# Optimization experiments

Measured on AMD Instinct MI355X. Metric: run time of the kernel, lower is better.

The kernel has to match this reference:

```python
import jax, jax.numpy as jnp
import numpy as np

PARENTS = np.array([-1, 0, 1, 1, 1])
NECK_CHAIN = np.array([1, 0])  # neck joint (1) up to root (0)
B, V, F, J, S, E = 512, 5023, 9976, 5, 100, 50
L_STAT, L_DYN, L_FULL, N_BUCKET = 51, 17, 68, 79


def rodrigues(rvec):
    """Axis-angle [N,3] -> rotation matrices [N,3,3]."""
    angle = jnp.linalg.norm(rvec + 1e-8, axis=-1, keepdims=True)  # [N,1]
    axis = rvec / angle
    s = jnp.sin(angle)[..., None]
    c = jnp.cos(angle)[..., None]
    rx, ry, rz = axis[:, 0], axis[:, 1], axis[:, 2]
    z = jnp.zeros_like(rx)
    K = jnp.stack([z, -rz, ry, rz, z, -rx, -ry, rx, z], axis=-1).reshape(-1, 3, 3)
    I = jnp.eye(3, dtype=rvec.dtype)
    return I + s * K + (1.0 - c) * (K @ K)


def verts2lmk(vertices, faces, lmk_faces_idx, lmk_bary):
    lmk_faces = faces[lmk_faces_idx]                               # [B,L,3]
    lmk_verts = jax.vmap(lambda v, f: v[f])(vertices, lmk_faces)   # [B,L,3verts,3xyz]
    return jnp.einsum('blfc,blf->blc', lmk_verts, lmk_bary)


def setup_inputs() -> dict:
    key = jax.random.key(0)
    ks = jax.random.split(key, 16)
    shape_params = jax.random.normal(ks[0], (B, S), jnp.float32)
    expression_params = jax.random.normal(ks[1], (B, E), jnp.float32)
    pose_params = 0.2 * jax.random.normal(ks[2], (B, 6), jnp.float32)
    eye_pose_params = 0.1 * jax.random.normal(ks[3], (B, 6), jnp.float32)
    v_template = jax.random.normal(ks[4], (V, 3), jnp.float32) * 0.1
    shapedirs = jax.random.normal(ks[5], (V, 3, S + E), jnp.float32) * 0.01
    posedirs = jax.random.normal(ks[6], ((J - 1) * 9, V * 3), jnp.float32) * 0.01
    jr = jax.random.uniform(ks[7], (J, V), jnp.float32)
    J_regressor = jr / jnp.sum(jr, axis=1, keepdims=True)
    lbs_weights = jax.nn.softmax(jax.random.normal(ks[8], (V, J), jnp.float32), axis=-1)
    faces = jax.random.randint(ks[9], (F, 3), 0, V)
    lmk_faces_idx = jax.random.randint(ks[10], (L_STAT,), 0, F)
    lb = jax.random.uniform(ks[11], (L_STAT, 3), jnp.float32) + 1e-3
    lmk_bary_coords = lb / jnp.sum(lb, axis=-1, keepdims=True)
    dynamic_lmk_faces_idx = jax.random.randint(ks[12], (N_BUCKET, L_DYN), 0, F)
    db = jax.random.uniform(ks[13], (N_BUCKET, L_DYN, 3), jnp.float32) + 1e-3
    dynamic_lmk_bary_coords = db / jnp.sum(db, axis=-1, keepdims=True)
    full_lmk_faces_idx = jax.random.randint(ks[14], (L_FULL,), 0, F)
    fb = jax.random.uniform(ks[15], (L_FULL, 3), jnp.float32) + 1e-3
    full_lmk_bary_coords = fb / jnp.sum(fb, axis=-1, keepdims=True)
    return {
        'shape_params': shape_params, 'expression_params': expression_params,
        'pose_params': pose_params, 'eye_pose_params': eye_pose_params,
        'v_template': v_template, 'shapedirs': shapedirs, 'posedirs': posedirs,
        'J_regressor': J_regressor, 'lbs_weights': lbs_weights, 'faces': faces,
        'lmk_faces_idx': lmk_faces_idx, 'lmk_bary_coords': lmk_bary_coords,
        'dynamic_lmk_faces_idx': dynamic_lmk_faces_idx,
        'dynamic_lmk_bary_coords': dynamic_lmk_bary_coords,
        'full_lmk_faces_idx': full_lmk_faces_idx,
        'full_lmk_bary_coords': full_lmk_bary_coords,
    }


def reference(shape_params, expression_params, pose_params, eye_pose_params,
              v_template, shapedirs, posedirs, J_regressor, lbs_weights, faces,
              lmk_faces_idx, lmk_bary_coords, dynamic_lmk_faces_idx,
              dynamic_lmk_bary_coords, full_lmk_faces_idx, full_lmk_bary_coords):
    b = shape_params.shape[0]
    nv = v_template.shape[0]
    dt = shape_params.dtype
    betas = jnp.concatenate([shape_params, expression_params], axis=1)          # [B,150]
    neck = jnp.zeros((b, 3), dtype=dt)
    full_pose = jnp.concatenate(
        [pose_params[:, :3], neck, pose_params[:, 3:], eye_pose_params], axis=1)  # [B,15]
    # shape + expression blendshapes
    v_shaped = v_template[None] + jnp.einsum('bl,vcl->bvc', betas, shapedirs)   # [B,V,3]
    joints = jnp.einsum('jv,bvc->bjc', J_regressor, v_shaped)                   # [B,5,3]
    rot_mats = rodrigues(full_pose.reshape(-1, 3)).reshape(b, J, 3, 3)          # [B,5,3,3]
    I3 = jnp.eye(3, dtype=dt)
    pose_feature = (rot_mats[:, 1:] - I3).reshape(b, -1)                        # [B,36]
    v_posed = v_shaped + (pose_feature @ posedirs).reshape(b, nv, 3)
    # kinematic chain -> global joint transforms
    rel_J = joints.at[:, 1:].add(-joints[:, PARENTS[1:]])
    tm = jnp.zeros((b, J, 4, 4), dtype=dt)
    tm = tm.at[:, :, :3, :3].set(rot_mats).at[:, :, :3, 3].set(rel_J).at[:, :, 3, 3].set(1.0)
    chain = [tm[:, 0]]
    for i in range(1, J):
        chain.append(chain[PARENTS[i]] @ tm[:, i])
    A = jnp.stack(chain, axis=1)                                                # [B,5,4,4]
    Rj = jnp.einsum('bjmn,bjn->bjm', A[:, :, :3, :3], joints)
    A_rel = A.at[:, :, :3, 3].add(-Rj)
    # per-vertex skinning
    T = jnp.einsum('vj,bjmn->bvmn', lbs_weights, A_rel)                         # [B,V,4,4]
    vertices = jnp.einsum('bvmn,bvn->bvm', T[:, :, :3, :3], v_posed) + T[:, :, :3, 3]
    # dynamic contour landmark selection from neck kin-chain relative rotation
    aa = full_pose.reshape(b, J, 3)[:, NECK_CHAIN]                              # [B,2,3]
    rc = rodrigues(aa.reshape(-1, 3)).reshape(b, len(NECK_CHAIN), 3, 3)
    rel_rot = jnp.broadcast_to(I3, (b, 3, 3))
    for idx in range(len(NECK_CHAIN)):
        rel_rot = rc[:, idx] @ rel_rot
    sy = jnp.sqrt(rel_rot[:, 0, 0] ** 2 + rel_rot[:, 1, 0] ** 2)
    y_deg = jnp.arctan2(-rel_rot[:, 2, 0], sy) * (180.0 / np.pi)
    y_rot = jnp.round(jnp.minimum(y_deg, 39.0)).astype(jnp.int32)
    neg_mask = y_rot < 0
    big_neg = y_rot < -39
    neg_vals = jnp.where(big_neg, 78, 39 - y_rot)
    y_rot = jnp.where(neg_mask, neg_vals, y_rot)                                # [B] in [0,79)
    dyn_faces = dynamic_lmk_faces_idx[y_rot]                                    # [B,17]
    dyn_bary = dynamic_lmk_bary_coords[y_rot]                                   # [B,17,3]
    lf = jnp.concatenate([dyn_faces, jnp.broadcast_to(lmk_faces_idx[None], (b, lmk_faces_idx.shape[0]))], axis=1)
    lb = jnp.concatenate([dyn_bary, jnp.broadcast_to(lmk_bary_coords[None], (b,) + lmk_bary_coords.shape)], axis=1)
    landmarks2d = verts2lmk(vertices, faces, lf, lb)
    ff = jnp.broadcast_to(full_lmk_faces_idx[None], (b, full_lmk_faces_idx.shape[0]))
    fb = jnp.broadcast_to(full_lmk_bary_coords[None], (b,) + full_lmk_bary_coords.shape)
    landmarks3d = verts2lmk(vertices, faces, ff, fb)
    return (vertices, landmarks2d, landmarks3d)
```

## Files before the change

kernel.cpp:

```cpp
#include <hip/hip_runtime.h>
#include <cstddef>
#include <cstdint>

#define cB   512
#define cV   5023
#define cS   100
#define cE   50
#define cJ   5
#define cLD  17
#define cLF  68

#define cV3    15069
#define cNPAD  15072

#define OUT_V  ((size_t)cB * cV * 3)
#define OUT_L  ((size_t)cB * cLF * 3)

#define WS_BTN    ((size_t)0)
#define WS_ATM    (WS_BTN + (size_t)cNPAD * 96)
#define WS_JS2    (WS_ATM + 49152)
#define WS_AREL   (WS_JS2 + 2432)
#define WS_YROT   (WS_AREL + 30720)
#define WS_JSPART (WS_YROT + 512)

typedef __attribute__((ext_vector_type(8))) short short8;
typedef __attribute__((ext_vector_type(4))) float f32x4;

__device__ __forceinline__ unsigned short f2bf(float x) {
  unsigned int u = __float_as_uint(x);
  u = (u + 0x7fffu + ((u >> 16) & 1u)) >> 16;
  return (unsigned short)u;
}

__device__ __forceinline__ void rodrigues9(float rx, float ry, float rz, float* R) {
  float a0 = rx + 1e-8f, a1 = ry + 1e-8f, a2 = rz + 1e-8f;
  float angle = sqrtf(a0 * a0 + a1 * a1 + a2 * a2);
  float inv = 1.0f / angle;
  float x = rx * inv, y = ry * inv, z = rz * inv;
  float s = sinf(angle), c = cosf(angle);
  float t = 1.0f - c;
  float xy = x * y, xz = x * z, yz = y * z;
  R[0] = 1.0f - t * (y * y + z * z);
  R[1] = -s * z + t * xy;
  R[2] =  s * y + t * xz;
  R[3] =  s * z + t * xy;
  R[4] = 1.0f - t * (x * x + z * z);
  R[5] = -s * x + t * yz;
  R[6] = -s * y + t * xz;
  R[7] =  s * x + t * yz;
  R[8] = 1.0f - t * (x * x + y * y);
}

__global__ __launch_bounds__(512) void k_aux(
    const float* __restrict__ sd, const float* __restrict__ pd,
    const float* __restrict__ jreg, const float* __restrict__ vt,
    unsigned int* __restrict__ btn_u, float* __restrict__ JSpart) {
  __shared__ __align__(16) unsigned char sm[44032];
  float* sdt = (float*)sm;
  unsigned short* pdt = (unsigned short*)(sm + 38912);
  const int t = threadIdx.x;
  const int bid = blockIdx.x;
  if (bid < 314) {
    if (t >= 453) return;
    int c = t / 151, l = t - c * 151;
    int v0 = bid * 16;
    float acc[5] = {0.f, 0.f, 0.f, 0.f, 0.f};
#pragma unroll 8
    for (int vi = 0; vi < 16; ++vi) {
      int v = v0 + vi;
      bool ok = (v < cV);
      int vc = ok ? v : 0;
      float x;
      if (l < 150) x = ok ? sd[(size_t)(v * 3 + c) * 150 + l] : 0.f;
      else         x = ok ? vt[v * 3 + c] : 0.f;
#pragma unroll
      for (int j = 0; j < 5; ++j)
        acc[j] = fmaf(jreg[j * cV + vc], x, acc[j]);
    }
#pragma unroll
    for (int j = 0; j < 5; ++j)
      JSpart[(size_t)bid * 2272 + (j * 3 + c) * 151 + l] = acc[j];
  } else {
    const int n0 = (bid - 314) * 64;
    for (int idx = t; idx < 9600; idx += 512) {
      size_t g = (size_t)n0 * 150 + idx;
      float v = (g < (size_t)cV3 * 150) ? sd[g] : 0.f;
      int row = idx / 150, col = idx - row * 150;
      sdt[row * 152 + col] = v;
    }
    for (int e = t; e < 2304; e += 512) {
      int kk = e >> 6, ln = e & 63;
      int n = n0 + ln;
      pdt[ln * 38 + kk] = f2bf((n < cV3) ? pd[(size_t)kk * cV3 + n] : 0.f);
    }
    __syncthreads();
    for (int e = t; e < 6144; e += 512) {
      int row = e / 96, d = e - row * 96;
      int n = n0 + row;
      if (n < cNPAD) {
        unsigned int wv;
        if (d < 75) {
          wv = (unsigned int)f2bf(sdt[row * 152 + 2 * d]) |
               ((unsigned int)f2bf(sdt[row * 152 + 2 * d + 1]) << 16);
        } else if (d < 93) {
          int p = (d - 75) * 2;
          wv = (unsigned int)pdt[row * 38 + p] |
               ((unsigned int)pdt[row * 38 + p + 1] << 16);
        } else {
          wv = 0u;
        }
        btn_u[(size_t)n * 96 + d] = wv;
      }
    }
  }
}

__global__ __launch_bounds__(256) void k_jsred(const float* __restrict__ JSpart,
                                               float* __restrict__ JS2) {
  __shared__ float red[256];
  const int t = threadIdx.x;
  const int e = blockIdx.x * 32 + (t & 31);
  const int pg = t >> 5;
  float s = 0.f;
  if (e < 2265) {
#pragma unroll 8
    for (int p = pg; p < 314; p += 8)
      s += JSpart[(size_t)p * 2272 + e];
  }
  red[t] = s;
  __syncthreads();
  if (t < 128) red[t] += red[t + 128];
  __syncthreads();
  if (t < 64) red[t] += red[t + 64];
  __syncthreads();
  if (t < 32) {
    float v = red[t] + red[t + 32];
    if (e < 2265) {
      int jc = e / 151, l = e - jc * 151;
      JS2[l * 16 + jc] = v;
    }
  }
}

__global__ __launch_bounds__(256) void k_batch(
    const float* __restrict__ shp, const float* __restrict__ expr,
    const float* __restrict__ pose, const float* __restrict__ eyep,
    const float* __restrict__ JS2g, float* __restrict__ Arel,
    int* __restrict__ yrot, unsigned int* __restrict__ atm_u) {
  __shared__ float js2[151 * 16];
  __shared__ float sb[32 * 153];
  __shared__ float pfs[32 * 36];
  const int t = threadIdx.x;
  const int b0 = blockIdx.x * 32;
  for (int i = t; i < 151 * 16; i += 256) js2[i] = JS2g[i];
  for (int e = t; e < 3200; e += 256) {
    int bl = e / 100, l = e - bl * 100;
    sb[bl * 153 + l] = shp[(size_t)(b0 + bl) * 100 + l];
  }
  for (int e = t; e < 1600; e += 256) {
    int bl = e / 50, l = e - bl * 50;
    sb[bl * 153 + 100 + l] = expr[(size_t)(b0 + bl) * 50 + l];
  }
  __syncthreads();

  if (t < 32) {
    int b = b0 + t;
    float jnt[5][3];
    {
      const f32x4* J4 = (const f32x4*)(js2 + 150 * 16);
      f32x4 A = J4[0], Bq = J4[1], Cq = J4[2], Dq = J4[3];
      jnt[0][0] = A.x;  jnt[0][1] = A.y;  jnt[0][2] = A.z;
      jnt[1][0] = A.w;  jnt[1][1] = Bq.x; jnt[1][2] = Bq.y;
      jnt[2][0] = Bq.z; jnt[2][1] = Bq.w; jnt[2][2] = Cq.x;
      jnt[3][0] = Cq.y; jnt[3][1] = Cq.z; jnt[3][2] = Cq.w;
      jnt[4][0] = Dq.x; jnt[4][1] = Dq.y; jnt[4][2] = Dq.z;
    }
    for (int l = 0; l < 150; ++l) {
      const f32x4* J4 = (const f32x4*)(js2 + l * 16);
      f32x4 A = J4[0], Bq = J4[1], Cq = J4[2], Dq = J4[3];
      float beta = sb[t * 153 + l];
      jnt[0][0] = fmaf(beta, A.x,  jnt[0][0]);
      jnt[0][1] = fmaf(beta, A.y,  jnt[0][1]);
      jnt[0][2] = fmaf(beta, A.z,  jnt[0][2]);
      jnt[1][0] = fmaf(beta, A.w,  jnt[1][0]);
      jnt[1][1] = fmaf(beta, Bq.x, jnt[1][1]);
      jnt[1][2] = fmaf(beta, Bq.y, jnt[1][2]);
      jnt[2][0] = fmaf(beta, Bq.z, jnt[2][0]);
      jnt[2][1] = fmaf(beta, Bq.w, jnt[2][1]);
      jnt[2][2] = fmaf(beta, Cq.x, jnt[2][2]);
      jnt[3][0] = fmaf(beta, Cq.y, jnt[3][0]);
      jnt[3][1] = fmaf(beta, Cq.z, jnt[3][1]);
      jnt[3][2] = fmaf(beta, Cq.w, jnt[3][2]);
      jnt[4][0] = fmaf(beta, Dq.x, jnt[4][0]);
      jnt[4][1] = fmaf(beta, Dq.y, jnt[4][1]);
      jnt[4][2] = fmaf(beta, Dq.z, jnt[4][2]);
    }
    float fp[5][3];
    fp[0][0] = pose[b * 6 + 0]; fp[0][1] = pose[b * 6 + 1]; fp[0][2] = pose[b * 6 + 2];
    fp[1][0] = 0.f; fp[1][1] = 0.f; fp[1][2] = 0.f;
    fp[2][0] = pose[b * 6 + 3]; fp[2][1] = pose[b * 6 + 4]; fp[2][2] = pose[b * 6 + 5];
    fp[3][0] = eyep[b * 6 + 0]; fp[3][1] = eyep[b * 6 + 1]; fp[3][2] = eyep[b * 6 + 2];
    fp[4][0] = eyep[b * 6 + 3]; fp[4][1] = eyep[b * 6 + 4]; fp[4][2] = eyep[b * 6 + 5];
    float R[5][9];
#pragma unroll
    for (int j = 0; j < 5; ++j) rodrigues9(fp[j][0], fp[j][1], fp[j][2], R[j]);
#pragma unroll
    for (int j = 1; j < 5; ++j)
#pragma unroll
      for (int r = 0; r < 9; ++r) {
        float id = (r == 0 || r == 4 || r == 8) ? 1.f : 0.f;
        pfs[t * 36 + (j - 1) * 9 + r] = R[j][r] - id;
      }
    float rel[5][3];
#pragma unroll
    for (int c = 0; c < 3; ++c) {
      rel[0][c] = jnt[0][c];
      rel[1][c] = jnt[1][c] - jnt[0][c];
      rel[2][c] = jnt[2][c] - jnt[1][c];
      rel[3][c] = jnt[3][c] - jnt[1][c];
      rel[4][c] = jnt[4][c] - jnt[1][c];
    }
    float GR[5][9], Gt[5][3];
#pragma unroll
    for (int r = 0; r < 9; ++r) GR[0][r] = R[0][r];
#pragma unroll
    for (int c = 0; c < 3; ++c) Gt[0][c] = rel[0][c];
    const int par[5] = {0, 0, 1, 1, 1};
#pragma unroll
    for (int j = 1; j < 5; ++j) {
      int p = par[j];
#pragma unroll
      for (int r = 0; r < 3; ++r) {
#pragma unroll
        for (int cc = 0; cc < 3; ++cc)
          GR[j][r * 3 + cc] = GR[p][r * 3 + 0] * R[j][0 + cc] +
                              GR[p][r * 3 + 1] * R[j][3 + cc] +
                              GR[p][r * 3 + 2] * R[j][6 + cc];
        Gt[j][r] = Gt[p][r] + GR[p][r * 3 + 0] * rel[j][0] +
                              GR[p][r * 3 + 1] * rel[j][1] +
                              GR[p][r * 3 + 2] * rel[j][2];
      }
    }
#pragma unroll
    for (int j = 0; j < 5; ++j)
#pragma unroll
      for (int r = 0; r < 3; ++r) {
        float tj = Gt[j][r] - (GR[j][r * 3 + 0] * jnt[j][0] +
                               GR[j][r * 3 + 1] * jnt[j][1] +
                               GR[j][r * 3 + 2] * jnt[j][2]);
        Arel[b * 60 + j * 12 + r * 4 + 0] = GR[j][r * 3 + 0];
        Arel[b * 60 + j * 12 + r * 4 + 1] = GR[j][r * 3 + 1];
        Arel[b * 60 + j * 12 + r * 4 + 2] = GR[j][r * 3 + 2];
        Arel[b * 60 + j * 12 + r * 4 + 3] = tj;
      }
    float Ra[9], Rb[9];
    rodrigues9(fp[1][0], fp[1][1], fp[1][2], Ra);
    rodrigues9(fp[0][0], fp[0][1], fp[0][2], Rb);
    float r00 = Rb[0] * Ra[0] + Rb[1] * Ra[3] + Rb[2] * Ra[6];
    float r10 = Rb[3] * Ra[0] + Rb[4] * Ra[3] + Rb[5] * Ra[6];
    float r20 = Rb[6] * Ra[0] + Rb[7] * Ra[3] + Rb[8] * Ra[6];
    float sy = sqrtf(r00 * r00 + r10 * r10);
    float ydeg = atan2f(-r20, sy) * 57.29577951308232f;
    int y = (int)rintf(fminf(ydeg, 39.0f));
    if (y < 0) y = (y < -39) ? 78 : (39 - y);
    yrot[b] = y;
  }
  __syncthreads();

#pragma unroll
  for (int it = 0; it < 12; ++it) {
    int e = t + it * 256;
    int bl = e / 96, d = e - bl * 96;
    unsigned int wv;
    if (d < 75) {
      wv = (unsigned int)f2bf(sb[bl * 153 + 2 * d]) |
           ((unsigned int)f2bf(sb[bl * 153 + 2 * d + 1]) << 16);
    } else if (d < 93) {
      wv = (unsigned int)f2bf(pfs[bl * 36 + (d - 75) * 2]) |
           ((unsigned int)f2bf(pfs[bl * 36 + (d - 75) * 2 + 1]) << 16);
    } else {
      wv = 0u;
    }
    atm_u[(size_t)(b0 + bl) * 96 + d] = wv;
  }
}

__global__ __launch_bounds__(256) void k_main(
    const unsigned short* __restrict__ BTn, const unsigned short* __restrict__ ATm,
    const float* __restrict__ Arel, const float* __restrict__ vtempl,
    const float* __restrict__ lbw, float* __restrict__ out) {
  __shared__ float Pf[96 * 66];
  __shared__ float Os[64 * 97];
  __shared__ float lbwT[160];
  __shared__ float vtT[96];

  const int bid = blockIdx.x;
  const int nb = bid >> 3, mb = bid & 7;

  const int t = threadIdx.x;
  const int w = t >> 6, L = t & 63;
  const int wm = w >> 1, wn = w & 1;
  const int lr = L & 15, lq = L >> 4;

  if (t < 160) {
    int vl = t / 5, j = t - vl * 5;
    int v = nb * 32 + vl;
    lbwT[t] = (v < cV) ? lbw[v * 5 + j] : 0.f;
  }
  if (t >= 160 && t < 256) {
    int e = t - 160;
    int vl = e / 3, c = e - vl * 3;
    int v = nb * 32 + vl;
    vtT[e] = (v < cV) ? vtempl[v * 3 + c] : 0.f;
  }

  const unsigned short* abase = ATm + ((size_t)mb * 64 + wm * 32 + lr) * 192 + lq * 8;
  const unsigned short* bbase = BTn + ((size_t)nb * 96 + wn * 48 + lr) * 192 + lq * 8;

  f32x4 acc[2][3];
#pragma unroll
  for (int mt = 0; mt < 2; ++mt)
#pragma unroll
    for (int nt = 0; nt < 3; ++nt) acc[mt][nt] = (f32x4){0.f, 0.f, 0.f, 0.f};

  short8 af0 = *(const short8*)(abase);
  short8 af1 = *(const short8*)(abase + 16 * 192);
  short8 bf0 = *(const short8*)(bbase);
  short8 bf1 = *(const short8*)(bbase + 16 * 192);
  short8 bf2 = *(const short8*)(bbase + 32 * 192);
#pragma unroll
  for (int ks = 0; ks < 6; ++ks) {
    short8 naf0, naf1, nbf0, nbf1, nbf2;
    if (ks < 5) {
      const int ko = (ks + 1) * 32;
      naf0 = *(const short8*)(abase + ko);
      naf1 = *(const short8*)(abase + 16 * 192 + ko);
      nbf0 = *(const short8*)(bbase + ko);
      nbf1 = *(const short8*)(bbase + 16 * 192 + ko);
      nbf2 = *(const short8*)(bbase + 32 * 192 + ko);
    }
    acc[0][0] = __builtin_amdgcn_mfma_f32_16x16x32_bf16(af0, bf0, acc[0][0], 0, 0, 0);
    acc[1][0] = __builtin_amdgcn_mfma_f32_16x16x32_bf16(af1, bf0, acc[1][0], 0, 0, 0);
    acc[0][1] = __builtin_amdgcn_mfma_f32_16x16x32_bf16(af0, bf1, acc[0][1], 0, 0, 0);
    acc[1][1] = __builtin_amdgcn_mfma_f32_16x16x32_bf16(af1, bf1, acc[1][1], 0, 0, 0);
    acc[0][2] = __builtin_amdgcn_mfma_f32_16x16x32_bf16(af0, bf2, acc[0][2], 0, 0, 0);
    acc[1][2] = __builtin_amdgcn_mfma_f32_16x16x32_bf16(af1, bf2, acc[1][2], 0, 0, 0);
    af0 = naf0; af1 = naf1; bf0 = nbf0; bf1 = nbf1; bf2 = nbf2;
  }

#pragma unroll
  for (int mt = 0; mt < 2; ++mt)
#pragma unroll
    for (int nt = 0; nt < 3; ++nt) {
      int n_loc = wn * 48 + nt * 16 + lr;
      int m = wm * 32 + mt * 16 + lq * 4;
      *(f32x4*)(Pf + n_loc * 66 + m) = acc[mt][nt];
    }

  const int b_loc = t >> 2, part = t & 3;
  const float* qb = Arel + ((size_t)mb * 64 + b_loc) * 60;
  f32x4 ar[15];
#pragma unroll
  for (int r = 0; r < 15; ++r) ar[r] = *(const f32x4*)(qb + 4 * r);

  __syncthreads();

#pragma unroll
  for (int ii = 0; ii < 8; ++ii) {
    const int vl = part * 8 + ii;
    float px = Pf[(vl * 3 + 0) * 66 + b_loc] + vtT[vl * 3 + 0];
    float py = Pf[(vl * 3 + 1) * 66 + b_loc] + vtT[vl * 3 + 1];
    float pz = Pf[(vl * 3 + 2) * 66 + b_loc] + vtT[vl * 3 + 2];
    float o0 = 0.f, o1 = 0.f, o2 = 0.f;
#pragma unroll
    for (int j = 0; j < 5; ++j) {
      f32x4 q0 = ar[3 * j + 0], q1 = ar[3 * j + 1], q2 = ar[3 * j + 2];
      float s0 = q0.x * px + q0.y * py + q0.z * pz + q0.w;
      float s1 = q1.x * px + q1.y * py + q1.z * pz + q1.w;
      float s2 = q2.x * px + q2.y * py + q2.z * pz + q2.w;
      float wj = lbwT[vl * 5 + j];
      o0 = fmaf(wj, s0, o0);
      o1 = fmaf(wj, s1, o1);
      o2 = fmaf(wj, s2, o2);
    }
    Os[b_loc * 97 + vl * 3 + 0] = o0;
    Os[b_loc * 97 + vl * 3 + 1] = o1;
    Os[b_loc * 97 + vl * 3 + 2] = o2;
  }
  __syncthreads();

  const size_t cv3 = (size_t)cV * 3;
  const size_t ob = ((size_t)(mb * 64) * cV + (size_t)nb * 32) * 3;
#pragma unroll
  for (int s = 0; s < 24; ++s) {
    int idx = s * 256 + t;
    int bb = idx / 96, f = idx - bb * 96;
    if (nb < 156 || f < 93)
      out[ob + (size_t)bb * cv3 + f] = Os[bb * 97 + f];
  }
}

__global__ __launch_bounds__(512) void k_lmk(
    const float* __restrict__ verts, const int* __restrict__ faces,
    const int* __restrict__ lmkf, const float* __restrict__ lmkb,
    const int* __restrict__ dynf, const float* __restrict__ dynb,
    const int* __restrict__ fullf, const float* __restrict__ fullb,
    const int* __restrict__ yrot, float* __restrict__ out) {
  int id = blockIdx.x * 512 + threadIdx.x;
  if (id >= cB * cLF * 6) return;
  int c = id % 3;
  int q = id / 3;
  int sel = q & 1;
  int r = q >> 1;
  int b = r / cLF, l = r - b * cLF;
  const float* vb = verts + (size_t)b * cV * 3;
  int f; float w0, w1, w2; size_t o;
  if (sel == 0) {
    if (l < cLD) {
      int yb = yrot[b];
      f = dynf[yb * cLD + l];
      const float* bp = dynb + ((size_t)yb * cLD + l) * 3;
      w0 = bp[0]; w1 = bp[1]; w2 = bp[2];
    } else {
      f = lmkf[l - cLD];
      const float* bp = lmkb + (size_t)(l - cLD) * 3;
      w0 = bp[0]; w1 = bp[1]; w2 = bp[2];
    }
    o = OUT_V + ((size_t)b * cLF + l) * 3;
  } else {
    f = fullf[l];
    const float* bp = fullb + (size_t)l * 3;
    w0 = bp[0]; w1 = bp[1]; w2 = bp[2];
    o = OUT_V + OUT_L + ((size_t)b * cLF + l) * 3;
  }
  int i0 = faces[f * 3 + 0] * 3, i1 = faces[f * 3 + 1] * 3, i2 = faces[f * 3 + 2] * 3;
  out[o + c] = w0 * vb[i0 + c] + w1 * vb[i1 + c] + w2 * vb[i2 + c];
}

extern "C" void kernel_launch(void* const* d_in, const int* in_sizes, int n_in,
                              void* d_out, int out_size, void* d_ws, size_t ws_size,
                              hipStream_t stream) {
  (void)in_sizes; (void)n_in; (void)out_size; (void)ws_size;
  const float* shp  = (const float*)d_in[0];
  const float* expr = (const float*)d_in[1];
  const float* pose = (const float*)d_in[2];
  const float* eyep = (const float*)d_in[3];
  const float* vt   = (const float*)d_in[4];
  const float* sd   = (const float*)d_in[5];
  const float* pd   = (const float*)d_in[6];
  const float* jreg = (const float*)d_in[7];
  const float* lbw  = (const float*)d_in[8];
  const int*   fcs  = (const int*)d_in[9];
  const int*   lmkf = (const int*)d_in[10];
  const float* lmkb = (const float*)d_in[11];
  const int*   dynf = (const int*)d_in[12];
  const float* dynb = (const float*)d_in[13];
  const int*   fullf= (const int*)d_in[14];
  const float* fullb= (const float*)d_in[15];
  float* out = (float*)d_out;
  float* ws  = (float*)d_ws;

  unsigned int*   btn  = (unsigned int*)(ws + WS_BTN);
  unsigned short* ATm  = (unsigned short*)(ws + WS_ATM);
  float* JS2    = ws + WS_JS2;
  float* Arel   = ws + WS_AREL;
  int*   yrot   = (int*)(ws + WS_YROT);
  float* JSpart = ws + WS_JSPART;

  k_aux<<<550, 512, 0, stream>>>(sd, pd, jreg, vt, btn, JSpart);
  k_jsred<<<71, 256, 0, stream>>>(JSpart, JS2);
  k_batch<<<16, 256, 0, stream>>>(shp, expr, pose, eyep, JS2, Arel, yrot,
                                  (unsigned int*)ATm);
  k_main<<<1256, 256, 0, stream>>>((unsigned short*)btn, ATm, Arel, vt, lbw, out);
  k_lmk<<<408, 512, 0, stream>>>(out, fcs, lmkf, lmkb, dynf, dynb, fullf, fullb, yrot, out);
}
```

Before: 174.8 us.

## Fuse joint-regressor partials into shapedir packing blocks and shrink main GEMM tiles

The aux kernel now has every block stage a 64-row shapedir tile in shared memory and reuse it both for the joint-regressor partial sums and for bf16 packing. This drops the separate 314 regressor blocks that re-read shapedirs from global memory. The main kernel becomes one wavefront per block computing a 64x48 MFMA tile with double-buffered fragments. Each lane then skins its own batch row and writes straight to global memory, so the shared-memory output staging and barriers are gone. The trade-off is uncoalesced strided stores (each lane writes a different batch row) and per-lane global loads of lbw and vtemplate.

```diff
diff --git a/kernel.cpp b/kernel.cpp
--- a/kernel.cpp
+++ b/kernel.cpp
@@ -55,62 +55,74 @@
     const float* __restrict__ sd, const float* __restrict__ pd,
     const float* __restrict__ jreg, const float* __restrict__ vt,
     unsigned int* __restrict__ btn_u, float* __restrict__ JSpart) {
-  __shared__ __align__(16) unsigned char sm[44032];
+  __shared__ __align__(16) unsigned char sm[44544];
   float* sdt = (float*)sm;
   unsigned short* pdt = (unsigned short*)(sm + 38912);
+  float* vtc = (float*)(sm + 43776);
+  float* jt  = (float*)(sm + 44032);
   const int t = threadIdx.x;
   const int bid = blockIdx.x;
-  if (bid < 314) {
-    if (t >= 453) return;
+  const int n0 = bid * 64;
+  const int v0 = n0 / 3;
+
+  for (int idx = t; idx < 9600; idx += 512) {
+    size_t g = (size_t)n0 * 150 + idx;
+    float v = (g < (size_t)cV3 * 150) ? sd[g] : 0.f;
+    int row = idx / 150, col = idx - row * 150;
+    sdt[row * 152 + col] = v;
+  }
+  for (int e = t; e < 2304; e += 512) {
+    int kk = e >> 6, ln = e & 63;
+    int n = n0 + ln;
+    pdt[ln * 38 + kk] = f2bf((n < cV3) ? pd[(size_t)kk * cV3 + n] : 0.f);
+  }
+  if (t < 64) {
+    int n = n0 + t;
+    vtc[t] = (n < cV3) ? vt[n] : 0.f;
+  }
+  if (t >= 64 && t < 174) {
+    int e = t - 64;
+    int j = e / 22, vi = e - j * 22;
+    int v = v0 + vi;
+    jt[j * 22 + vi] = (v < cV) ? jreg[j * cV + v] : 0.f;
+  }
+  __syncthreads();
+
+  if (t < 453) {
     int c = t / 151, l = t - c * 151;
-    int v0 = bid * 16;
+    const int base = 3 * v0 + c - n0;
     float acc[5] = {0.f, 0.f, 0.f, 0.f, 0.f};
-#pragma unroll 8
-    for (int vi = 0; vi < 16; ++vi) {
-      int v = v0 + vi;
-      bool ok = (v < cV);
-      int vc = ok ? v : 0;
-      float x;
-      if (l < 150) x = ok ? sd[(size_t)(v * 3 + c) * 150 + l] : 0.f;
-      else         x = ok ? vt[v * 3 + c] : 0.f;
-#pragma unroll
-      for (int j = 0; j < 5; ++j)
-        acc[j] = fmaf(jreg[j * cV + vc], x, acc[j]);
+#pragma unroll
+    for (int vi = 0; vi < 22; ++vi) {
+      int r = base + 3 * vi;
+      if (r >= 0 && r < 64) {
+        float x = (l < 150) ? sdt[r * 152 + l] : vtc[r];
+#pragma unroll
+        for (int j = 0; j < 5; ++j)
+          acc[j] = fmaf(jt[j * 22 + vi], x, acc[j]);
+      }
     }
 #pragma unroll
     for (int j = 0; j < 5; ++j)
       JSpart[(size_t)bid * 2272 + (j * 3 + c) * 151 + l] = acc[j];
-  } else {
-    const int n0 = (bid - 314) * 64;
-    for (int idx = t; idx < 9600; idx += 512) {
-      size_t g = (size_t)n0 * 150 + idx;
-      float v = (g < (size_t)cV3 * 150) ? sd[g] : 0.f;
-      int row = idx / 150, col = idx - row * 150;
-      sdt[row * 152 + col] = v;
-    }
-    for (int e = t; e < 2304; e += 512) {
-      int kk = e >> 6, ln = e & 63;
-      int n = n0 + ln;
-      pdt[ln * 38 + kk] = f2bf((n < cV3) ? pd[(size_t)kk * cV3 + n] : 0.f);
-    }
-    __syncthreads();
-    for (int e = t; e < 6144; e += 512) {
-      int row = e / 96, d = e - row * 96;
-      int n = n0 + row;
-      if (n < cNPAD) {
-        unsigned int wv;
-        if (d < 75) {
-          wv = (unsigned int)f2bf(sdt[row * 152 + 2 * d]) |
-               ((unsigned int)f2bf(sdt[row * 152 + 2 * d + 1]) << 16);
-        } else if (d < 93) {
-          int p = (d - 75) * 2;
-          wv = (unsigned int)pdt[row * 38 + p] |
-               ((unsigned int)pdt[row * 38 + p + 1] << 16);
-        } else {
-          wv = 0u;
-        }
-        btn_u[(size_t)n * 96 + d] = wv;
-      }
+  }
+
+  for (int e = t; e < 6144; e += 512) {
+    int row = e / 96, d = e - row * 96;
+    int n = n0 + row;
+    if (n < cNPAD) {
+      unsigned int wv;
+      if (d < 75) {
+        wv = (unsigned int)f2bf(sdt[row * 152 + 2 * d]) |
+             ((unsigned int)f2bf(sdt[row * 152 + 2 * d + 1]) << 16);
+      } else if (d < 93) {
+        int p = (d - 75) * 2;
+        wv = (unsigned int)pdt[row * 38 + p] |
+             ((unsigned int)pdt[row * 38 + p + 1] << 16);
+      } else {
+        wv = 0u;
+      }
+      btn_u[(size_t)n * 96 + d] = wv;
     }
   }
 }
@@ -124,7 +136,7 @@
   float s = 0.f;
   if (e < 2265) {
 #pragma unroll 8
-    for (int p = pg; p < 314; p += 8)
+    for (int p = pg; p < 236; p += 8)
       s += JSpart[(size_t)p * 2272 + e];
   }
   red[t] = s;
@@ -285,118 +297,92 @@
   }
 }
 
-__global__ __launch_bounds__(256) void k_main(
+__global__ __launch_bounds__(64) void k_main(
     const unsigned short* __restrict__ BTn, const unsigned short* __restrict__ ATm,
     const float* __restrict__ Arel, const float* __restrict__ vtempl,
     const float* __restrict__ lbw, float* __restrict__ out) {
-  __shared__ float Pf[96 * 66];
-  __shared__ float Os[64 * 97];
-  __shared__ float lbwT[160];
-  __shared__ float vtT[96];
+  __shared__ float Pf[48 * 66];
 
   const int bid = blockIdx.x;
   const int nb = bid >> 3, mb = bid & 7;
-
-  const int t = threadIdx.x;
-  const int w = t >> 6, L = t & 63;
-  const int wm = w >> 1, wn = w & 1;
+  const int L = threadIdx.x;
   const int lr = L & 15, lq = L >> 4;
 
-  if (t < 160) {
-    int vl = t / 5, j = t - vl * 5;
-    int v = nb * 32 + vl;
-    lbwT[t] = (v < cV) ? lbw[v * 5 + j] : 0.f;
-  }
-  if (t >= 160 && t < 256) {
-    int e = t - 160;
-    int vl = e / 3, c = e - vl * 3;
-    int v = nb * 32 + vl;
-    vtT[e] = (v < cV) ? vtempl[v * 3 + c] : 0.f;
-  }
-
-  const unsigned short* abase = ATm + ((size_t)mb * 64 + wm * 32 + lr) * 192 + lq * 8;
-  const unsigned short* bbase = BTn + ((size_t)nb * 96 + wn * 48 + lr) * 192 + lq * 8;
-
-  f32x4 acc[2][3];
-#pragma unroll
-  for (int mt = 0; mt < 2; ++mt)
+  const unsigned short* abase = ATm + ((size_t)mb * 64 + lr) * 192 + lq * 8;
+  const unsigned short* bbase = BTn + ((size_t)nb * 48 + lr) * 192 + lq * 8;
+
+  f32x4 acc[4][3];
+#pragma unroll
+  for (int mt = 0; mt < 4; ++mt)
 #pragma unroll
     for (int nt = 0; nt < 3; ++nt) acc[mt][nt] = (f32x4){0.f, 0.f, 0.f, 0.f};
 
-  short8 af0 = *(const short8*)(abase);
-  short8 af1 = *(const short8*)(abase + 16 * 192);
-  short8 bf0 = *(const short8*)(bbase);
-  short8 bf1 = *(const short8*)(bbase + 16 * 192);
-  short8 bf2 = *(const short8*)(bbase + 32 * 192);
+  short8 Ar[2][4], Br[2][3];
+#pragma unroll
+  for (int mt = 0; mt < 4; ++mt) Ar[0][mt] = *(const short8*)(abase + mt * 16 * 192);
+#pragma unroll
+  for (int nt = 0; nt < 3; ++nt) Br[0][nt] = *(const short8*)(bbase + nt * 16 * 192);
+
 #pragma unroll
   for (int ks = 0; ks < 6; ++ks) {
-    short8 naf0, naf1, nbf0, nbf1, nbf2;
+    const int cur = ks & 1, nxt = cur ^ 1;
     if (ks < 5) {
       const int ko = (ks + 1) * 32;
-      naf0 = *(const short8*)(abase + ko);
-      naf1 = *(const short8*)(abase + 16 * 192 + ko);
-      nbf0 = *(const short8*)(bbase + ko);
-      nbf1 = *(const short8*)(bbase + 16 * 192 + ko);
-      nbf2 = *(const short8*)(bbase + 32 * 192 + ko);
-    }
-    acc[0][0] = __builtin_amdgcn_mfma_f32_16x16x32_bf16(af0, bf0, acc[0][0], 0, 0, 0);
-    acc[1][0] = __builtin_amdgcn_mfma_f32_16x16x32_bf16(af1, bf0, acc[1][0], 0, 0, 0);
-    acc[0][1] = __builtin_amdgcn_mfma_f32_16x16x32_bf16(af0, bf1, acc[0][1], 0, 0, 0);
-    acc[1][1] = __builtin_amdgcn_mfma_f32_16x16x32_bf16(af1, bf1, acc[1][1], 0, 0, 0);
-    acc[0][2] = __builtin_amdgcn_mfma_f32_16x16x32_bf16(af0, bf2, acc[0][2], 0, 0, 0);
-    acc[1][2] = __builtin_amdgcn_mfma_f32_16x16x32_bf16(af1, bf2, acc[1][2], 0, 0, 0);
-    af0 = naf0; af1 = naf1; bf0 = nbf0; bf1 = nbf1; bf2 = nbf2;
-  }
-
-#pragma unroll
-  for (int mt = 0; mt < 2; ++mt)
+#pragma unroll
+      for (int mt = 0; mt < 4; ++mt)
+        Ar[nxt][mt] = *(const short8*)(abase + mt * 16 * 192 + ko);
+#pragma unroll
+      for (int nt = 0; nt < 3; ++nt)
+        Br[nxt][nt] = *(const short8*)(bbase + nt * 16 * 192 + ko);
+    }
+#pragma unroll
+    for (int nt = 0; nt < 3; ++nt)
+#pragma unroll
+      for (int mt = 0; mt < 4; ++mt)
+        acc[mt][nt] = __builtin_amdgcn_mfma_f32_16x16x32_bf16(
+            Ar[cur][mt], Br[cur][nt], acc[mt][nt], 0, 0, 0);
+  }
+
+#pragma unroll
+  for (int mt = 0; mt < 4; ++mt)
 #pragma unroll
     for (int nt = 0; nt < 3; ++nt) {
-      int n_loc = wn * 48 + nt * 16 + lr;
-      int m = wm * 32 + mt * 16 + lq * 4;
+      int n_loc = nt * 16 + lr;
+      int m = mt * 16 + lq * 4;
       *(f32x4*)(Pf + n_loc * 66 + m) = acc[mt][nt];
     }
 
-  const int b_loc = t >> 2, part = t & 3;
-  const float* qb = Arel + ((size_t)mb * 64 + b_loc) * 60;
+  const int b = mb * 64 + L;
+  const float* qb = Arel + (size_t)b * 60;
   f32x4 ar[15];
 #pragma unroll
   for (int r = 0; r < 15; ++r) ar[r] = *(const f32x4*)(qb + 4 * r);
 
-  __syncthreads();
-
-#pragma unroll
-  for (int ii = 0; ii < 8; ++ii) {
-    const int vl = part * 8 + ii;
-    float px = Pf[(vl * 3 + 0) * 66 + b_loc] + vtT[vl * 3 + 0];
-    float py = Pf[(vl * 3 + 1) * 66 + b_loc] + vtT[vl * 3 + 1];
-    float pz = Pf[(vl * 3 + 2) * 66 + b_loc] + vtT[vl * 3 + 2];
-    float o0 = 0.f, o1 = 0.f, o2 = 0.f;
-#pragma unroll
-    for (int j = 0; j < 5; ++j) {
-      f32x4 q0 = ar[3 * j + 0], q1 = ar[3 * j + 1], q2 = ar[3 * j + 2];
-      float s0 = q0.x * px + q0.y * py + q0.z * pz + q0.w;
-      float s1 = q1.x * px + q1.y * py + q1.z * pz + q1.w;
-      float s2 = q2.x * px + q2.y * py + q2.z * pz + q2.w;
-      float wj = lbwT[vl * 5 + j];
-      o0 = fmaf(wj, s0, o0);
-      o1 = fmaf(wj, s1, o1);
-      o2 = fmaf(wj, s2, o2);
-    }
-    Os[b_loc * 97 + vl * 3 + 0] = o0;
-    Os[b_loc * 97 + vl * 3 + 1] = o1;
-    Os[b_loc * 97 + vl * 3 + 2] = o2;
-  }
-  __syncthreads();
-
-  const size_t cv3 = (size_t)cV * 3;
-  const size_t ob = ((size_t)(mb * 64) * cV + (size_t)nb * 32) * 3;
-#pragma unroll
-  for (int s = 0; s < 24; ++s) {
-    int idx = s * 256 + t;
-    int bb = idx / 96, f = idx - bb * 96;
-    if (nb < 156 || f < 93)
-      out[ob + (size_t)bb * cv3 + f] = Os[bb * 97 + f];
+  const int vg0 = nb * 16;
+  float* ob = out + ((size_t)b * cV + vg0) * 3;
+#pragma unroll
+  for (int vl = 0; vl < 16; ++vl) {
+    const int v = vg0 + vl;
+    if (v < cV) {
+      float px = Pf[(vl * 3 + 0) * 66 + L] + vtempl[v * 3 + 0];
+      float py = Pf[(vl * 3 + 1) * 66 + L] + vtempl[v * 3 + 1];
+      float pz = Pf[(vl * 3 + 2) * 66 + L] + vtempl[v * 3 + 2];
+      float o0 = 0.f, o1 = 0.f, o2 = 0.f;
+#pragma unroll
+      for (int j = 0; j < 5; ++j) {
+        f32x4 q0 = ar[3 * j + 0], q1 = ar[3 * j + 1], q2 = ar[3 * j + 2];
+        float s0 = q0.x * px + q0.y * py + q0.z * pz + q0.w;
+        float s1 = q1.x * px + q1.y * py + q1.z * pz + q1.w;
+        float s2 = q2.x * px + q2.y * py + q2.z * pz + q2.w;
+        float wj = lbw[v * 5 + j];
+        o0 = fmaf(wj, s0, o0);
+        o1 = fmaf(wj, s1, o1);
+        o2 = fmaf(wj, s2, o2);
+      }
+      ob[vl * 3 + 0] = o0;
+      ob[vl * 3 + 1] = o1;
+      ob[vl * 3 + 2] = o2;
+    }
   }
 }
 
@@ -467,10 +453,10 @@
   int*   yrot   = (int*)(ws + WS_YROT);
   float* JSpart = ws + WS_JSPART;
 
-  k_aux<<<550, 512, 0, stream>>>(sd, pd, jreg, vt, btn, JSpart);
+  k_aux<<<236, 512, 0, stream>>>(sd, pd, jreg, vt, btn, JSpart);
   k_jsred<<<71, 256, 0, stream>>>(JSpart, JS2);
   k_batch<<<16, 256, 0, stream>>>(shp, expr, pose, eyep, JS2, Arel, yrot,
                                   (unsigned int*)ATm);
-  k_main<<<1256, 256, 0, stream>>>((unsigned short*)btn, ATm, Arel, vt, lbw, out);
+  k_main<<<2512, 64, 0, stream>>>((unsigned short*)btn, ATm, Arel, vt, lbw, out);
   k_lmk<<<408, 512, 0, stream>>>(out, fcs, lmkf, lmkb, dynf, dynb, fullf, fullb, yrot, out);
 }
```

After: 187.7 us. 7.4% more time.
